# Performance work log

Measured on AMD Instinct MI355X. Metric: run time of the kernel, lower is better.

Reference implementation:

```python
import jax, jax.numpy as jnp
import numpy as np

B, DIM, H, W = 512, 256, 14, 14
HEADS, KD, VD = 4, 16, 64  # key_dim=16, val_dim=attn_ratio*key_dim=64
RES = 14


def _bn(x, g, b, rm, rv, eps=1e-5):
    # eval-mode BatchNorm2d folded into per-channel affine
    s = g / jnp.sqrt(rv + eps)
    return x * s[None, :, None, None] + (b - rm * s)[None, :, None, None]


def setup_inputs() -> dict:
    key = jax.random.key(0)
    ks = jax.random.split(key, 6)
    # relative position bias index table: offset (|dy|,|dx|) -> flat index
    ii = np.arange(RES * RES)
    ry, rx = ii // RES, ii % RES
    dyo = np.abs(ry[:, None] - ry[None, :])
    dxo = np.abs(rx[:, None] - rx[None, :])
    bias_idxs = jnp.asarray(dyo * RES + dxo, dtype=jnp.int32)  # [196,196]
    QKV_OUT = 2 * KD + VD  # 96
    inp = {
        'x': jax.random.normal(ks[0], (B, DIM, H, W), jnp.float32),
        'qkv_w': jax.random.normal(ks[1], (HEADS, QKV_OUT, DIM // HEADS), jnp.float32) * 0.05,
        'qkv_g': jnp.ones((HEADS, QKV_OUT), jnp.float32),
        'qkv_b': jnp.zeros((HEADS, QKV_OUT), jnp.float32),
        'qkv_rm': jnp.zeros((HEADS, QKV_OUT), jnp.float32),
        'qkv_rv': jnp.ones((HEADS, QKV_OUT), jnp.float32),
        'dw_w': jax.random.normal(ks[2], (HEADS, KD, 1, 5, 5), jnp.float32) * 0.05,
        'dw_g': jnp.ones((HEADS, KD), jnp.float32),
        'dw_b': jnp.zeros((HEADS, KD), jnp.float32),
        'dw_rm': jnp.zeros((HEADS, KD), jnp.float32),
        'dw_rv': jnp.ones((HEADS, KD), jnp.float32),
        'proj_w': jax.random.normal(ks[3], (DIM, VD * HEADS), jnp.float32) * 0.05,
        'proj_g': jnp.ones((DIM,), jnp.float32),
        'proj_b': jnp.zeros((DIM,), jnp.float32),
        'proj_rm': jnp.zeros((DIM,), jnp.float32),
        'proj_rv': jnp.ones((DIM,), jnp.float32),
        'attn_biases': jax.random.normal(ks[4], (HEADS, RES * RES), jnp.float32) * 0.02,
        'bias_idxs': bias_idxs,
    }
    return inp


def reference(x, qkv_w, qkv_g, qkv_b, qkv_rm, qkv_rv,
              dw_w, dw_g, dw_b, dw_rm, dw_rv,
              proj_w, proj_g, proj_b, proj_rm, proj_rv,
              attn_biases, bias_idxs):
    Bc, C, Hc, Wc = x.shape
    N = Hc * Wc
    scale = KD ** -0.5
    bias = attn_biases[:, bias_idxs]  # [HEADS, N, N]
    chunks = jnp.split(x, HEADS, axis=1)  # per-head [B, dim//heads, H, W]
    feat = chunks[0]
    outs = []
    for h in range(HEADS):  # cascading residual -> inherently sequential over heads
        if h > 0:
            feat = feat + chunks[h]
        f = jnp.einsum('oc,bchw->bohw', qkv_w[h], feat)  # 1x1 conv
        f = _bn(f, qkv_g[h], qkv_b[h], qkv_rm[h], qkv_rv[h])
        q, k, v = f[:, :KD], f[:, KD:2 * KD], f[:, 2 * KD:]
        # 5x5 depthwise conv on q, padding 2
        q = jax.lax.conv_general_dilated(
            q, dw_w[h], window_strides=(1, 1), padding=[(2, 2), (2, 2)],
            dimension_numbers=('NCHW', 'OIHW', 'NCHW'), feature_group_count=KD)
        q = _bn(q, dw_g[h], dw_b[h], dw_rm[h], dw_rv[h])
        qf = q.reshape(Bc, KD, N) * scale
        kf = k.reshape(Bc, KD, N)
        vf = v.reshape(Bc, VD, N)
        attn = jnp.einsum('bdn,bdm->bnm', qf, kf) + bias[h]  # [B, N, N]
        attn = jax.nn.softmax(attn, axis=-1)
        feat = jnp.einsum('bdm,bnm->bdn', vf, attn).reshape(Bc, VD, Hc, Wc)
        outs.append(feat)
    y = jax.nn.relu(jnp.concatenate(outs, axis=1))  # [B, VD*HEADS, H, W]
    y = jnp.einsum('oc,bchw->bohw', proj_w, y)
    return _bn(y, proj_g, proj_b, proj_rm, proj_rv)
```

## Files before the change

kernel.cpp:

```cpp
#include <hip/hip_runtime.h>
#include <math.h>

#define BATCH 512
#define DIM 256
#define HEADS 4
#define KD 16
#define VD 64
#define NQ 196
#define CHW (DIM * NQ)

typedef __attribute__((ext_vector_type(8))) short short8;
typedef __attribute__((ext_vector_type(4))) float f32x4;

#define MFMA16(A, B, C) __builtin_amdgcn_mfma_f32_16x16x32_bf16((A), (B), (C), 0, 0, 0)

__device__ __forceinline__ unsigned short f2bf(float f) {
    unsigned int u = __float_as_uint(f);
    u += 0x7FFFu + ((u >> 16) & 1u);
    return (unsigned short)(u >> 16);
}
__device__ __forceinline__ float bf2f(unsigned short h) {
    return __uint_as_float(((unsigned int)h) << 16);
}

#define OFF_QC    0
#define OFF_P0    16640
#define OFF_P1    33280
#define OFF_QRAW  49920
#define OFF_KB1   63232
#define OFF_KB2   81152
#define OFF_VBH   99072
#define OFF_VBL   128768
#define OFF_DEN4  158464
#define OFF_SB    161792
#define OFF_TB    162176
#define OFF_DWS   162560
#define OFF_DWT   162624
#define SMEM_BYTES 162688

__global__ __launch_bounds__(256)
void prep_kernel(const float* __restrict__ attn_biases,
                 const int* __restrict__ bias_idxs,
                 const float* __restrict__ qkv_w,
                 const float* __restrict__ proj_w,
                 float* __restrict__ biasg,
                 unsigned short* __restrict__ whH,
                 unsigned short* __restrict__ whL,
                 unsigned short* __restrict__ pwH,
                 unsigned short* __restrict__ pwL) {
    int i = blockIdx.x * 256 + threadIdx.x;
    const int T1 = HEADS * NQ * NQ;
    const int T2 = HEADS * 96 * 64;
    const int T3 = DIM * DIM;
    if (i < T1) {
        int h = i / (NQ * NQ);
        int r = i - h * (NQ * NQ);
        biasg[i] = attn_biases[h * NQ + bias_idxs[r]];
    } else if (i < T1 + T2) {
        int j = i - T1;
        float v = qkv_w[j];
        unsigned short hh = f2bf(v);
        whH[j] = hh;
        whL[j] = f2bf(v - bf2f(hh));
    } else if (i < T1 + T2 + T3) {
        int j = i - T1 - T2;
        float v = proj_w[j];
        unsigned short hh = f2bf(v);
        pwH[j] = hh;
        pwL[j] = f2bf(v - bf2f(hh));
    }
}

__global__ __launch_bounds__(1024, 4)
void cascade_attn_kernel(const float* __restrict__ x,
                         const unsigned short* __restrict__ whH,
                         const unsigned short* __restrict__ whL,
                         const float* __restrict__ qkv_g,
                         const float* __restrict__ qkv_b,
                         const float* __restrict__ qkv_rm,
                         const float* __restrict__ qkv_rv,
                         const float* __restrict__ dw_w,
                         const float* __restrict__ dw_g,
                         const float* __restrict__ dw_b,
                         const float* __restrict__ dw_rm,
                         const float* __restrict__ dw_rv,
                         const float* __restrict__ biasg,
                         unsigned short* __restrict__ yrelu) {
    extern __shared__ __align__(16) char smem[];
    unsigned short* featU = (unsigned short*)(smem + OFF_QC);
    unsigned short* qc    = (unsigned short*)(smem + OFF_QC);
    unsigned short* Pb0   = (unsigned short*)(smem + OFF_P0);
    unsigned short* Pb1   = (unsigned short*)(smem + OFF_P1);
    float*          qraw  = (float*)(smem + OFF_QRAW);
    unsigned short* kb1   = (unsigned short*)(smem + OFF_KB1);
    unsigned short* kb2   = (unsigned short*)(smem + OFF_KB2);
    unsigned short* vbH   = (unsigned short*)(smem + OFF_VBH);
    unsigned short* vbL   = (unsigned short*)(smem + OFF_VBL);
    float*          den4  = (float*)(smem + OFF_DEN4);
    float*          sbT   = (float*)(smem + OFF_SB);
    float*          tbT   = (float*)(smem + OFF_TB);
    float*          dwsT  = (float*)(smem + OFF_DWS);
    float*          dwtT  = (float*)(smem + OFF_DWT);

    const int b    = blockIdx.x;
    const int tid  = threadIdx.x;
    const int w    = tid >> 6;
    const int li   = tid & 15;
    const int quad = (tid >> 4) & 3;
    const int tn0  = tid % NQ;
    const int tc0  = tid / NQ;

    for (int t = tid; t < SMEM_BYTES / 4; t += 1024) ((unsigned int*)smem)[t] = 0u;
    __syncthreads();
    for (int t = tid; t < VD * NQ; t += 1024) {
        int n = t % NQ, c = t / NQ;
        featU[n * 72 + c] = f2bf(x[((size_t)b * DIM + c) * NQ + n]);
    }
    __syncthreads();

    for (int h = 0; h < HEADS; ++h) {
        if (tid < 96) {
            float s = qkv_g[h * 96 + tid] * rsqrtf(qkv_rv[h * 96 + tid] + 1e-5f);
            sbT[tid] = s;
            tbT[tid] = qkv_b[h * 96 + tid] - qkv_rm[h * 96 + tid] * s;
        } else if (tid < 112) {
            int c = tid - 96;
            float s = dw_g[h * 16 + c] * rsqrtf(dw_rv[h * 16 + c] + 1e-5f);
            dwsT[c] = s;
            dwtT[c] = dw_b[h * 16 + c] - dw_rm[h * 16 + c] * s;
        }
        __syncthreads();

        for (int T = w; T < 78; T += 16) {
            int ot = T / 13, nt = T - ot * 13;
            const size_t wb = ((size_t)h * 96 + ot * 16 + li) * 64;
            short8 ah0 = *(const short8*)(whH + wb + quad * 8);
            short8 al0 = *(const short8*)(whL + wb + quad * 8);
            short8 ah1 = *(const short8*)(whH + wb + 32 + quad * 8);
            short8 al1 = *(const short8*)(whL + wb + 32 + quad * 8);
            short8 b0 = *(const short8*)(featU + (nt * 16 + li) * 72 + quad * 8);
            short8 b1 = *(const short8*)(featU + (nt * 16 + li) * 72 + 32 + quad * 8);
            f32x4 acc = {0.f, 0.f, 0.f, 0.f};
            acc = MFMA16(ah0, b0, acc);
            acc = MFMA16(al0, b0, acc);
            acc = MFMA16(ah1, b1, acc);
            acc = MFMA16(al1, b1, acc);
            int n = nt * 16 + li;
            bool nok = (n < NQ);
            #pragma unroll
            for (int r = 0; r < 4; ++r) {
                int o = ot * 16 + quad * 4 + r;
                float val = acc[r] * sbT[o] + tbT[o];
                if (nok) {
                    if (o < 16) {
                        qraw[o * 208 + n] = val;
                    } else if (o < 32) {
                        int c = o - 16;
                        unsigned short hh = f2bf(val);
                        kb1[n * 40 + c] = hh;
                        kb1[n * 40 + 16 + c] = hh;
                        kb2[n * 40 + c] = f2bf(val - bf2f(hh));
                    } else {
                        int d = o - 32;
                        unsigned short hh = f2bf(val);
                        vbH[d * 232 + n] = hh;
                        vbL[d * 232 + n] = f2bf(val - bf2f(hh));
                    }
                }
            }
        }
        __syncthreads();

        {
            int n = tn0, c = tc0, py = tn0 / 14, px = tn0 - (tn0 / 14) * 14;
            for (int t = tid; t < KD * NQ; t += 1024) {
                const float* qr = qraw + c * 208;
                const float* wdc = dw_w + ((size_t)h * KD + c) * 25;
                float accv = 0.f;
                #pragma unroll
                for (int ky = 0; ky < 5; ++ky) {
                    int yy = py + ky - 2;
                    if (yy < 0 || yy >= 14) continue;
                    #pragma unroll
                    for (int kx = 0; kx < 5; ++kx) {
                        int xx = px + kx - 2;
                        if (xx < 0 || xx >= 14) continue;
                        accv = fmaf(wdc[ky * 5 + kx], qr[yy * 14 + xx], accv);
                    }
                }
                float val = fmaf(accv, dwsT[c], dwtT[c]) * 0.25f;
                unsigned short hh = f2bf(val);
                qc[n * 40 + c] = hh;
                qc[n * 40 + 16 + c] = f2bf(val - bf2f(hh));
                n += 44; c += 5; px += 2; py += 3;
                if (px >= 14) { px -= 14; ++py; }
                if (n >= NQ) { n -= NQ; ++c; py -= 14; }
            }
        }
        if (tid < 832) den4[tid] = 0.f;
        __syncthreads();

        f32x4 pacc[4];
        #pragma unroll
        for (int s = 0; s < 4; ++s) pacc[s] = (f32x4){0.f, 0.f, 0.f, 0.f};

        auto spass = [&](int mi2, unsigned short* __restrict__ PbW) {
            for (int T = w; T < 26; T += 16) {
                int s = (T >= 13) ? 1 : 0;
                int nt = T - s * 13;
                int n0 = nt * 16;
                int mg = mi2 * 32 + s * 16 + li;
                bool mok = (mg < NQ);
                float bias4[4];
                #pragma unroll
                for (int r = 0; r < 4; ++r) {
                    int n = n0 + quad * 4 + r;
                    int ni = n < NQ ? n : NQ - 1;
                    int mgi = mg < NQ ? mg : NQ - 1;
                    bias4[r] = biasg[(size_t)h * (NQ * NQ) + ni * NQ + mgi];
                }
                short8 q  = *(const short8*)(qc  + (n0 + li) * 40 + quad * 8);
                short8 k1 = *(const short8*)(kb1 + mg * 40 + quad * 8);
                short8 k2 = *(const short8*)(kb2 + mg * 40 + quad * 8);
                f32x4 acc = {0.f, 0.f, 0.f, 0.f};
                acc = MFMA16(q, k1, acc);
                acc = MFMA16(q, k2, acc);
                #pragma unroll
                for (int r = 0; r < 4; ++r) {
                    float e = mok ? __expf(acc[r] + bias4[r]) : 0.f;
                    PbW[(n0 + quad * 4 + r) * 40 + s * 16 + li] = f2bf(e);
                }
            }
        };

        spass(0, Pb0);
        __syncthreads();

        for (int mi = 0; mi < 7; ++mi) {
            unsigned short* PbR = (mi & 1) ? Pb1 : Pb0;
            unsigned short* PbW = (mi & 1) ? Pb0 : Pb1;
            if (mi < 6) spass(mi + 1, PbW);

            if (tid < 832) {
                int n = tid >> 2, part = tid & 3;
                short8 pv = *(const short8*)(PbR + n * 40 + part * 8);
                float sum = 0.f;
                #pragma unroll
                for (int j = 0; j < 8; ++j) sum += bf2f((unsigned short)pv[j]);
                den4[n * 4 + part] += sum;
            }
            #pragma unroll
            for (int slot = 0; slot < 4; ++slot) {
                int T = w + slot * 16;
                if (T < 52) {
                    int dt = T / 13, nt = T - dt * 13;
                    short8 p  = *(const short8*)(PbR + (nt * 16 + li) * 40 + quad * 8);
                    short8 vh = *(const short8*)(vbH + (dt * 16 + li) * 232 + mi * 32 + quad * 8);
                    short8 vl = *(const short8*)(vbL + (dt * 16 + li) * 232 + mi * 32 + quad * 8);
                    pacc[slot] = MFMA16(p, vh, pacc[slot]);
                    pacc[slot] = MFMA16(p, vl, pacc[slot]);
                }
            }
            __syncthreads();
        }

        #pragma unroll
        for (int slot = 0; slot < 4; ++slot) {
            int T = w + slot * 16;
            if (T < 52) {
                int dt = T / 13, nt = T - dt * 13;
                int d = dt * 16 + li;
                #pragma unroll
                for (int r = 0; r < 4; ++r) {
                    int n = nt * 16 + quad * 4 + r;
                    if (n < NQ) {
                        f32x4 dv = *(const f32x4*)(den4 + n * 4);
                        float dn = (dv.x + dv.y) + (dv.z + dv.w);
                        float val = pacc[slot][r] / dn;
                        featU[n * 72 + d] = f2bf(val);
                    }
                }
            }
        }
        __syncthreads();

        for (int t = tid; t < (VD * NQ) / 8; t += 1024) {
            int n  = t >> 3;
            int c0 = (t & 7) * 8;
            short8 u = *(const short8*)(featU + n * 72 + c0);
            short8 ru;
            #pragma unroll
            for (int j = 0; j < 8; ++j) {
                unsigned short uu = (unsigned short)u[j];
                ru[j] = (short)((uu & 0x8000u) ? (unsigned short)0 : uu);
            }
            *(short8*)(yrelu + ((size_t)b * NQ + n) * DIM + h * VD + c0) = ru;
        }
        __syncthreads();

        if (h < 3) {
            for (int t = tid; t < VD * NQ; t += 1024) {
                int n = t % NQ, c = t / NQ;
                float v = bf2f(featU[n * 72 + c]) + x[((size_t)b * DIM + (h + 1) * VD + c) * NQ + n];
                featU[n * 72 + c] = f2bf(v);
            }
            for (int t = tid; t < 12 * 64; t += 1024)
                featU[(NQ + t / 64) * 72 + (t & 63)] = 0;
        }
        __syncthreads();
    }
}

__global__ __launch_bounds__(512, 4)
void proj_kernel(const unsigned short* __restrict__ X,
                 const unsigned short* __restrict__ pwH,
                 const unsigned short* __restrict__ pwL,
                 const float* __restrict__ pg,
                 const float* __restrict__ pb,
                 const float* __restrict__ prm,
                 const float* __restrict__ prv,
                 float* __restrict__ out) {
    __shared__ __align__(16) unsigned short Xs[2][128 * 40];
    const int tid  = threadIdx.x;
    const int w    = tid >> 6;
    const int li   = tid & 15;
    const int quad = (tid >> 4) & 3;
    const int jb   = blockIdx.x * 128;

    const int jl = tid >> 2;
    const int c0 = (tid & 3) * 8;
    const unsigned short* xsrc = X + (size_t)(jb + jl) * 256 + c0;

    f32x4 acc[2][8];
    #pragma unroll
    for (int ot = 0; ot < 2; ++ot)
        #pragma unroll
        for (int jt = 0; jt < 8; ++jt) acc[ot][jt] = (f32x4){0.f, 0.f, 0.f, 0.f};

    *(short8*)(&Xs[0][jl * 40 + c0]) = *(const short8*)(xsrc);
    __syncthreads();

    const unsigned short* pH = pwH + (size_t)(w * 32 + li) * 256 + quad * 8;
    const unsigned short* pL = pwL + (size_t)(w * 32 + li) * 256 + quad * 8;

    for (int ks = 0; ks < 8; ++ks) {
        const int cur = ks & 1;
        short8 nv;
        if (ks < 7) nv = *(const short8*)(xsrc + (ks + 1) * 32);
        short8 ah0 = *(const short8*)(pH + ks * 32);
        short8 al0 = *(const short8*)(pL + ks * 32);
        short8 ah1 = *(const short8*)(pH + 16 * 256 + ks * 32);
        short8 al1 = *(const short8*)(pL + 16 * 256 + ks * 32);
        #pragma unroll
        for (int jt = 0; jt < 8; ++jt) {
            short8 bx = *(const short8*)(&Xs[cur][(jt * 16 + li) * 40 + quad * 8]);
            acc[0][jt] = MFMA16(ah0, bx, acc[0][jt]);
            acc[0][jt] = MFMA16(al0, bx, acc[0][jt]);
            acc[1][jt] = MFMA16(ah1, bx, acc[1][jt]);
            acc[1][jt] = MFMA16(al1, bx, acc[1][jt]);
        }
        if (ks < 7) {
            *(short8*)(&Xs[cur ^ 1][jl * 40 + c0]) = nv;
            __syncthreads();
        }
    }

    #pragma unroll
    for (int ot = 0; ot < 2; ++ot) {
        #pragma unroll
        for (int r = 0; r < 4; ++r) {
            int o = w * 32 + ot * 16 + quad * 4 + r;
            float s = pg[o] * rsqrtf(prv[o] + 1e-5f);
            float t = pb[o] - prm[o] * s;
            #pragma unroll
            for (int jt = 0; jt < 8; ++jt) {
                int j = jb + jt * 16 + li;
                int bb = j / NQ;
                int n = j - bb * NQ;
                out[(size_t)bb * CHW + (size_t)o * NQ + n] = fmaf(acc[ot][jt][r], s, t);
            }
        }
    }
}

extern "C" void kernel_launch(void* const* d_in, const int* in_sizes, int n_in,
                              void* d_out, int out_size, void* d_ws, size_t ws_size,
                              hipStream_t stream) {
    const float* x        = (const float*)d_in[0];
    const float* qkv_w    = (const float*)d_in[1];
    const float* qkv_g    = (const float*)d_in[2];
    const float* qkv_b    = (const float*)d_in[3];
    const float* qkv_rm   = (const float*)d_in[4];
    const float* qkv_rv   = (const float*)d_in[5];
    const float* dw_w     = (const float*)d_in[6];
    const float* dw_g     = (const float*)d_in[7];
    const float* dw_b     = (const float*)d_in[8];
    const float* dw_rm    = (const float*)d_in[9];
    const float* dw_rv    = (const float*)d_in[10];
    const float* proj_w   = (const float*)d_in[11];
    const float* proj_g   = (const float*)d_in[12];
    const float* proj_b   = (const float*)d_in[13];
    const float* proj_rm  = (const float*)d_in[14];
    const float* proj_rv  = (const float*)d_in[15];
    const float* attn_bs  = (const float*)d_in[16];
    const int*   bias_idx = (const int*)d_in[17];

    char* ws = (char*)d_ws;
    float* biasg = (float*)ws;
    unsigned short* yrelu = (unsigned short*)(ws + 614656);
    unsigned short* whH = (unsigned short*)(ws + 51994880);
    unsigned short* whL = (unsigned short*)(ws + 52044032);
    unsigned short* pwH = (unsigned short*)(ws + 52093184);
    unsigned short* pwL = (unsigned short*)(ws + 52224256);

    {
        int total = HEADS * NQ * NQ + HEADS * 96 * 64 + DIM * DIM;
        hipLaunchKernelGGL(prep_kernel, dim3((total + 255) / 256), dim3(256),
                           0, stream, attn_bs, bias_idx, qkv_w, proj_w,
                           biasg, whH, whL, pwH, pwL);
    }
    hipLaunchKernelGGL(cascade_attn_kernel, dim3(BATCH), dim3(1024),
                       SMEM_BYTES, stream,
                       x, whH, whL, qkv_g, qkv_b, qkv_rm, qkv_rv,
                       dw_w, dw_g, dw_b, dw_rm, dw_rv, biasg, yrelu);
    hipLaunchKernelGGL(proj_kernel, dim3(784), dim3(512), 0, stream,
                       yrelu, pwH, pwL, proj_g, proj_b, proj_rm, proj_rv,
                       (float*)d_out);
}
```

Baseline: 562.9 us.

## Fuse output projection into cascade attention kernel per batch

Removes the separate projection kernel and runs the 1x1 output projection plus BN at the end of each per-batch attention block, reading the block's own ReLU output back from global memory through double-buffered shared tiles. Each of the 16 waves computes 16 output channels across 13 column tiles that cover the 196 positions. This saves a kernel launch and lets the projection read recently written data that may still be in cache. In exchange, the padded 208-column tiles waste MFMA work, the epilogue lengthens the already long per-block kernel, and correctness depends on a __threadfence_block plus barrier making the global yrelu writes visible within the block.

```diff
diff --git a/kernel.cpp b/kernel.cpp
--- a/kernel.cpp
+++ b/kernel.cpp
@@ -85,7 +85,14 @@
                          const float* __restrict__ dw_rm,
                          const float* __restrict__ dw_rv,
                          const float* __restrict__ biasg,
-                         unsigned short* __restrict__ yrelu) {
+                         unsigned short* __restrict__ yrelu,
+                         const unsigned short* __restrict__ pwH,
+                         const unsigned short* __restrict__ pwL,
+                         const float* __restrict__ pg,
+                         const float* __restrict__ pb,
+                         const float* __restrict__ prm,
+                         const float* __restrict__ prv,
+                         float* __restrict__ out) {
     extern __shared__ __align__(16) char smem[];
     unsigned short* featU = (unsigned short*)(smem + OFF_QC);
     unsigned short* qc    = (unsigned short*)(smem + OFF_QC);
@@ -309,75 +316,59 @@
         }
         __syncthreads();
     }
-}
-
-__global__ __launch_bounds__(512, 4)
-void proj_kernel(const unsigned short* __restrict__ X,
-                 const unsigned short* __restrict__ pwH,
-                 const unsigned short* __restrict__ pwL,
-                 const float* __restrict__ pg,
-                 const float* __restrict__ pb,
-                 const float* __restrict__ prm,
-                 const float* __restrict__ prv,
-                 float* __restrict__ out) {
-    __shared__ __align__(16) unsigned short Xs[2][128 * 40];
-    const int tid  = threadIdx.x;
-    const int w    = tid >> 6;
-    const int li   = tid & 15;
-    const int quad = (tid >> 4) & 3;
-    const int jb   = blockIdx.x * 128;
-
-    const int jl = tid >> 2;
-    const int c0 = (tid & 3) * 8;
-    const unsigned short* xsrc = X + (size_t)(jb + jl) * 256 + c0;
-
-    f32x4 acc[2][8];
-    #pragma unroll
-    for (int ot = 0; ot < 2; ++ot)
+
+    {
+        __threadfence_block();
+        unsigned short* ych0 = Pb0;
+        unsigned short* ych1 = Pb1;
+        const int sn = tid >> 2;
+        const int sc = (tid & 3) * 8;
+        const unsigned short* ysrc = yrelu + ((size_t)b * NQ + sn) * DIM + sc;
+        const short8 z8 = {0, 0, 0, 0, 0, 0, 0, 0};
+
+        if (sn < NQ)       *(short8*)(ych0 + sn * 40 + sc) = *(const short8*)(ysrc);
+        else if (sn < 208) *(short8*)(ych0 + sn * 40 + sc) = z8;
+        __syncthreads();
+
+        const int o0 = w * 16;
+        const unsigned short* pHb = pwH + (size_t)(o0 + li) * 256 + quad * 8;
+        const unsigned short* pLb = pwL + (size_t)(o0 + li) * 256 + quad * 8;
+
+        f32x4 acc[13];
         #pragma unroll
-        for (int jt = 0; jt < 8; ++jt) acc[ot][jt] = (f32x4){0.f, 0.f, 0.f, 0.f};
-
-    *(short8*)(&Xs[0][jl * 40 + c0]) = *(const short8*)(xsrc);
-    __syncthreads();
-
-    const unsigned short* pH = pwH + (size_t)(w * 32 + li) * 256 + quad * 8;
-    const unsigned short* pL = pwL + (size_t)(w * 32 + li) * 256 + quad * 8;
-
-    for (int ks = 0; ks < 8; ++ks) {
-        const int cur = ks & 1;
-        short8 nv;
-        if (ks < 7) nv = *(const short8*)(xsrc + (ks + 1) * 32);
-        short8 ah0 = *(const short8*)(pH + ks * 32);
-        short8 al0 = *(const short8*)(pL + ks * 32);
-        short8 ah1 = *(const short8*)(pH + 16 * 256 + ks * 32);
-        short8 al1 = *(const short8*)(pL + 16 * 256 + ks * 32);
+        for (int nt = 0; nt < 13; ++nt) acc[nt] = (f32x4){0.f, 0.f, 0.f, 0.f};
+
         #pragma unroll
-        for (int jt = 0; jt < 8; ++jt) {
-            short8 bx = *(const short8*)(&Xs[cur][(jt * 16 + li) * 40 + quad * 8]);
-            acc[0][jt] = MFMA16(ah0, bx, acc[0][jt]);
-            acc[0][jt] = MFMA16(al0, bx, acc[0][jt]);
-            acc[1][jt] = MFMA16(ah1, bx, acc[1][jt]);
-            acc[1][jt] = MFMA16(al1, bx, acc[1][jt]);
-        }
-        if (ks < 7) {
-            *(short8*)(&Xs[cur ^ 1][jl * 40 + c0]) = nv;
-            __syncthreads();
-        }
-    }
-
-    #pragma unroll
-    for (int ot = 0; ot < 2; ++ot) {
+        for (int ks = 0; ks < 8; ++ks) {
+            unsigned short* cur = (ks & 1) ? ych1 : ych0;
+            unsigned short* nxt = (ks & 1) ? ych0 : ych1;
+            short8 nv;
+            if (ks < 7 && sn < NQ) nv = *(const short8*)(ysrc + (ks + 1) * 32);
+            short8 ah = *(const short8*)(pHb + ks * 32);
+            short8 al = *(const short8*)(pLb + ks * 32);
+            #pragma unroll
+            for (int nt = 0; nt < 13; ++nt) {
+                short8 bx = *(const short8*)(cur + (nt * 16 + li) * 40 + quad * 8);
+                acc[nt] = MFMA16(ah, bx, acc[nt]);
+                acc[nt] = MFMA16(al, bx, acc[nt]);
+            }
+            if (ks < 7) {
+                if (sn < NQ)       *(short8*)(nxt + sn * 40 + sc) = nv;
+                else if (sn < 208) *(short8*)(nxt + sn * 40 + sc) = z8;
+                __syncthreads();
+            }
+        }
+
         #pragma unroll
         for (int r = 0; r < 4; ++r) {
-            int o = w * 32 + ot * 16 + quad * 4 + r;
+            int o = o0 + quad * 4 + r;
             float s = pg[o] * rsqrtf(prv[o] + 1e-5f);
             float t = pb[o] - prm[o] * s;
             #pragma unroll
-            for (int jt = 0; jt < 8; ++jt) {
-                int j = jb + jt * 16 + li;
-                int bb = j / NQ;
-                int n = j - bb * NQ;
-                out[(size_t)bb * CHW + (size_t)o * NQ + n] = fmaf(acc[ot][jt][r], s, t);
+            for (int nt = 0; nt < 13; ++nt) {
+                int n = nt * 16 + li;
+                if (n < NQ)
+                    out[(size_t)b * CHW + (size_t)o * NQ + n] = fmaf(acc[nt][r], s, t);
             }
         }
     }
@@ -422,8 +413,7 @@
     hipLaunchKernelGGL(cascade_attn_kernel, dim3(BATCH), dim3(1024),
                        SMEM_BYTES, stream,
                        x, whH, whL, qkv_g, qkv_b, qkv_rm, qkv_rv,
-                       dw_w, dw_g, dw_b, dw_rm, dw_rv, biasg, yrelu);
-    hipLaunchKernelGGL(proj_kernel, dim3(784), dim3(512), 0, stream,
-                       yrelu, pwH, pwL, proj_g, proj_b, proj_rm, proj_rv,
+                       dw_w, dw_g, dw_b, dw_rm, dw_rv, biasg, yrelu,
+                       pwH, pwL, proj_g, proj_b, proj_rm, proj_rv,
                        (float*)d_out);
 }
```

Result: faster. 549.1 us (-2.5%).
